# Optimization experiments

Measured on AMD Instinct MI355X. Metric: run time of the kernel, lower is better.

The kernel has to match this reference:

```python
import jax, jax.numpy as jnp
import numpy as np

HEAD_SIZE = 64


def setup_inputs() -> dict:
    key = jax.random.key(0)
    k1, k2, k3, k4 = jax.random.split(key, 4)
    B, T, E = 8, 2048, 1024
    x = jax.random.normal(k1, (B, T, E), dtype=jnp.float32)
    # nn.Linear(n_embd, head_size, bias=False) weights: [head_size, n_embd]
    s = 1.0 / np.sqrt(E)
    Wk = jax.random.uniform(k2, (HEAD_SIZE, E), jnp.float32, -s, s)
    Wq = jax.random.uniform(k3, (HEAD_SIZE, E), jnp.float32, -s, s)
    Wv = jax.random.uniform(k4, (HEAD_SIZE, E), jnp.float32, -s, s)
    return {"x": x, "Wk": Wk, "Wq": Wq, "Wv": Wv}


def reference(x, Wk, Wq, Wv):
    # x: [B, T, E]; W*: [D, E] with D = head_size
    B, T, E = x.shape
    k = jnp.einsum("bte,de->btd", x, Wk)  # [B,T,D]
    q = jnp.einsum("bte,de->btd", x, Wq)
    v = jnp.einsum("bte,de->btd", x, Wv)
    scale = k.shape[-1] ** -0.5
    wei = jnp.einsum("btd,bsd->bts", q, k) * scale  # [B,T,T]
    causal = jnp.tril(jnp.ones((T, T), dtype=bool))
    wei = jnp.where(causal, wei, -jnp.inf)
    wei = jax.nn.softmax(wei, axis=-1)
    # dropout p=0.0 (eval): identity
    return jnp.einsum("bts,bsd->btd", wei, v)
```

## Files before the change

### kernel.cpp

```cpp
#include <hip/hip_runtime.h>
#include <hip/hip_bf16.h>


typedef __bf16 bf16x8 __attribute__((ext_vector_type(8)));
typedef float  f32x4  __attribute__((ext_vector_type(4)));

#define T_SEQ 2048
#define E_DIM 1024
#define D_HEAD 64
#define M_TOT 16384
#define NSPLIT 4
#define SC_LOG2E 0.18033688011112042f

#define BAR() asm volatile("s_barrier" ::: "memory")
#define WAITVM(N) do { asm volatile("s_waitcnt vmcnt(" #N ")" ::: "memory"); \
                       __builtin_amdgcn_sched_barrier(0); } while (0)

__device__ __forceinline__ unsigned short f2b(float f) {
  union { float f; unsigned int u; } cv; cv.f = f;
  unsigned int u = cv.u;
  u += 0x7FFFu + ((u >> 16) & 1u);
  return (unsigned short)(u >> 16);
}

__device__ __forceinline__ unsigned int f2b2(float a, float b) {
#if __has_builtin(__builtin_amdgcn_cvt_pk_bf16_f32)
  typedef __bf16 bf16x2_t __attribute__((ext_vector_type(2)));
  union { bf16x2_t v; unsigned int u; } cv;
  cv.v = __builtin_amdgcn_cvt_pk_bf16_f32(a, b);
  return cv.u;
#else
  return (unsigned int)f2b(a) | ((unsigned int)f2b(b) << 16);
#endif
}

__device__ __forceinline__ void dma16(const void* g, void* l) {
  __builtin_amdgcn_global_load_lds(
      (const __attribute__((address_space(1))) void*)g,
      (__attribute__((address_space(3))) void*)l, 16, 0, 0);
}

__global__ __launch_bounds__(256) void wcvt_kernel(
    const float* __restrict__ Wk, const float* __restrict__ Wq,
    const float* __restrict__ Wv, unsigned short* __restrict__ Wb)
{
  int i = blockIdx.x * 256 + threadIdx.x;
  int n = i >> 8, c4 = i & 255;
  const float* src = (n < 64) ? Wq + n * E_DIM
                   : (n < 128) ? Wk + (n - 64) * E_DIM
                               : Wv + (n - 128) * E_DIM;
  float4 v = *(const float4*)(src + c4 * 4);
  *(uint2*)(Wb + (size_t)n * E_DIM + c4 * 4) = make_uint2(f2b2(v.x, v.y), f2b2(v.z, v.w));
}

__global__ __launch_bounds__(256, 2) void proj_kernel(
    const float* __restrict__ x, const unsigned short* __restrict__ Wb,
    unsigned short* __restrict__ qws, unsigned short* __restrict__ kws,
    unsigned short* __restrict__ vtws)
{
  __shared__ __align__(16) float x_lds[2][32 * 64];
  __shared__ __align__(16) unsigned short w_lds[2][192 * 64];

  const int tid = threadIdx.x, wv = tid >> 6, lane = tid & 63;
  const int c = lane & 15, quad = lane >> 4;
  const int row0 = blockIdx.x * 32;

  auto stage = [&](int k0, int buf) {
    for (int j = 0; j < 2; ++j) {
      int base = (wv * 2 + j) * 64;
      int ci = base + lane;
      int r = ci >> 4, p = ci & 15, g = p ^ (r & 15);
      dma16(x + (size_t)(row0 + r) * E_DIM + k0 + g * 4, &x_lds[buf][base * 4]);
    }
    for (int j = 0; j < 6; ++j) {
      int base_r = (wv * 6 + j) * 8;
      int r = base_r + (lane >> 3);
      int g = (lane & 7) ^ (r & 7);
      dma16(Wb + (size_t)r * E_DIM + k0 + g * 8, &w_lds[buf][base_r * 64]);
    }
  };

  f32x4 acc[6];
  for (int j = 0; j < 6; ++j)
    for (int r = 0; r < 4; ++r) acc[j][r] = 0.0f;

  stage(0, 0);

  for (int s = 0; s < 16; ++s) {
    const int cur = s & 1;
    BAR();
    if (s < 15) { stage((s + 1) * 64, cur ^ 1); WAITVM(8); }
    else        { WAITVM(0); }
    BAR();

    for (int ks = 0; ks < 2; ++ks) {
      const int g0 = ks * 8 + quad * 2;
      union { unsigned int u[4]; bf16x8 v; } A0, A1;
      {
        const int m = c;
        f32x4 v1 = *(const f32x4*)&x_lds[cur][m * 64 + ((g0 ^ (m & 15)) << 2)];
        f32x4 v2 = *(const f32x4*)&x_lds[cur][m * 64 + (((g0 + 1) ^ (m & 15)) << 2)];
        A0.u[0] = f2b2(v1[0], v1[1]); A0.u[1] = f2b2(v1[2], v1[3]);
        A0.u[2] = f2b2(v2[0], v2[1]); A0.u[3] = f2b2(v2[2], v2[3]);
      }
      {
        const int m = 16 + c;
        f32x4 v1 = *(const f32x4*)&x_lds[cur][m * 64 + ((g0 ^ (m & 15)) << 2)];
        f32x4 v2 = *(const f32x4*)&x_lds[cur][m * 64 + (((g0 + 1) ^ (m & 15)) << 2)];
        A1.u[0] = f2b2(v1[0], v1[1]); A1.u[1] = f2b2(v1[2], v1[3]);
        A1.u[2] = f2b2(v2[0], v2[1]); A1.u[3] = f2b2(v2[2], v2[3]);
      }
      for (int j = 0; j < 3; ++j) {
        const int n = (wv * 3 + j) * 16 + c;
        bf16x8 bb = *(const bf16x8*)&w_lds[cur][n * 64 + (((ks * 4 + quad) ^ (n & 7)) << 3)];
        acc[j * 2]     = __builtin_amdgcn_mfma_f32_16x16x32_bf16(A0.v, bb, acc[j * 2], 0, 0, 0);
        acc[j * 2 + 1] = __builtin_amdgcn_mfma_f32_16x16x32_bf16(A1.v, bb, acc[j * 2 + 1], 0, 0, 0);
      }
    }
  }

  for (int mt = 0; mt < 2; ++mt) {
    const int rbase = row0 + mt * 16 + quad * 4;
    for (int j = 0; j < 3; ++j) {
      const int nt = wv * 3 + j;
      const f32x4 a = acc[j * 2 + mt];
      if (nt < 4) {
        int d = nt * 16 + c;
        for (int r = 0; r < 4; ++r)
          qws[(size_t)(rbase + r) * D_HEAD + d] = f2b(a[r] * SC_LOG2E);
      } else if (nt < 8) {
        int d = (nt - 4) * 16 + c;
        for (int r = 0; r < 4; ++r)
          kws[(size_t)(rbase + r) * D_HEAD + d] = f2b(a[r]);
      } else {
        int d = (nt - 8) * 16 + c;
        int bb = rbase >> 11, tt = rbase & 2047;
        *(ushort4*)&vtws[(size_t)bb * D_HEAD * T_SEQ + (size_t)d * T_SEQ + tt] =
            make_ushort4(f2b(a[0]), f2b(a[1]), f2b(a[2]), f2b(a[3]));
      }
    }
  }
}

__global__ __launch_bounds__(256, 4) void attn_kernel(
    const unsigned short* __restrict__ qws, const unsigned short* __restrict__ kws,
    const unsigned short* __restrict__ vtws,
    unsigned short* __restrict__ opart, float* __restrict__ lpart)
{
  __shared__ __align__(16) unsigned short k_lds[2 * 64 * 64];
  __shared__ __align__(16) unsigned short v_lds[2 * 64 * 64];
  __shared__ __align__(16) unsigned short p_lds[64 * 64];

  const int tid = threadIdx.x, wv = tid >> 6, lane = tid & 63;
  const int c = lane & 15, quad = lane >> 4;
  const int qi = blockIdx.x, b = blockIdx.y, sg = blockIdx.z;
  const int qt = ((sg ^ b) & 1) ? qi : 31 - qi;
  const int t0 = qt * 64;
  const size_t qkb = (size_t)b * T_SEQ * D_HEAD;
  const size_t vtb = (size_t)b * D_HEAD * T_SEQ;
  const int niter = (qt >= sg) ? ((qt - sg) >> 2) + 1 : 0;
  if (niter == 0) return;

  const int rloc = wv * 16 + quad * 4;
  const size_t prow = ((size_t)sg * 8 + b) * T_SEQ;

  const int mrow = wv * 16 + c;
  const bf16x8 qf0 = *(const bf16x8*)(qws + qkb + (size_t)(t0 + mrow) * D_HEAD + quad * 8);
  const bf16x8 qf1 = *(const bf16x8*)(qws + qkb + (size_t)(t0 + mrow) * D_HEAD + 32 + quad * 8);

  bf16x8 ones;
  { union { unsigned short s[8]; bf16x8 v; } o;
    for (int i = 0; i < 8; ++i) o.s[i] = 0x3F80;
    ones = o.v; }

  f32x4 acc_o[4], acc_l;
  for (int r = 0; r < 4; ++r) acc_l[r] = 0.0f;
  for (int nt = 0; nt < 4; ++nt)
    for (int r = 0; r < 4; ++r) acc_o[nt][r] = 0.0f;

  auto stageKV = [&](int s0, int buf) {
    unsigned short* kb = k_lds + buf * 4096;
    unsigned short* vb = v_lds + buf * 4096;
    for (int j = 0; j < 2; ++j) {
      int base = (wv * 2 + j) * 64;
      int p = base + lane;
      int r = p >> 3, g = (p & 7) ^ (r & 7);
      dma16(kws + qkb + (size_t)(s0 + r) * D_HEAD + g * 8, kb + base * 8);
    }
    for (int j = 0; j < 2; ++j) {
      int base = (wv * 2 + j) * 64;
      int p = base + lane;
      int r = p >> 3, g = (p & 7) ^ (r & 7);
      dma16(vtws + vtb + (size_t)r * T_SEQ + s0 + g * 8, vb + base * 8);
    }
  };

  const bool mydiag = (sg == (qt & 3));
  stageKV(sg * 64, 0);

  for (int it = 0; it < niter; ++it) {
    const int s0 = (sg + 4 * it) * 64;
    const int cur = it & 1;
    BAR();
    if (it + 1 < niter) { stageKV((sg + 4 * (it + 1)) * 64, cur ^ 1); WAITVM(4); }
    else                { WAITVM(0); }
    BAR();

    const unsigned short* kb = k_lds + cur * 4096;
    const unsigned short* vb = v_lds + cur * 4096;

    f32x4 accs[4];
    for (int nt = 0; nt < 4; ++nt)
      for (int r = 0; r < 4; ++r) accs[nt][r] = 0.0f;
    for (int nt = 0; nt < 4; ++nt) {
      int n = nt * 16 + c;
      bf16x8 kf0 = *(const bf16x8*)&kb[n * 64 + ((quad ^ (n & 7)) << 3)];
      bf16x8 kf1 = *(const bf16x8*)&kb[n * 64 + (((4 + quad) ^ (n & 7)) << 3)];
      accs[nt] = __builtin_amdgcn_mfma_f32_16x16x32_bf16(qf0, kf0, accs[nt], 0, 0, 0);
      accs[nt] = __builtin_amdgcn_mfma_f32_16x16x32_bf16(qf1, kf1, accs[nt], 0, 0, 0);
    }
    if (mydiag && it == niter - 1) {
      for (int nt = 0; nt < 4; ++nt) {
        int scol = s0 + nt * 16 + c;
        for (int r = 0; r < 4; ++r)
          if (scol > t0 + rloc + r) accs[nt][r] = -__builtin_inff();
      }
    }

    for (int nt = 0; nt < 4; ++nt)
      for (int r = 0; r < 4; ++r)
        accs[nt][r] = __builtin_exp2f(accs[nt][r]);

    for (int nt = 0; nt < 4; ++nt) {
      unsigned int u01 = f2b2(accs[nt][0], accs[nt][1]);
      unsigned int u23 = f2b2(accs[nt][2], accs[nt][3]);
      const int X = nt * 2 + (c >> 3), cl = c & 7;
      const int r0 = rloc, r1 = rloc + 1, r2 = rloc + 2, r3 = rloc + 3;
      p_lds[r0 * 64 + ((X ^ (r0 & 7)) << 3) + cl] = (unsigned short)u01;
      p_lds[r1 * 64 + ((X ^ (r1 & 7)) << 3) + cl] = (unsigned short)(u01 >> 16);
      p_lds[r2 * 64 + ((X ^ (r2 & 7)) << 3) + cl] = (unsigned short)u23;
      p_lds[r3 * 64 + ((X ^ (r3 & 7)) << 3) + cl] = (unsigned short)(u23 >> 16);
    }

    for (int ks = 0; ks < 2; ++ks) {
      int kg = ks * 4 + quad;
      bf16x8 pf = *(const bf16x8*)&p_lds[mrow * 64 + ((kg ^ (mrow & 7)) << 3)];
      acc_l = __builtin_amdgcn_mfma_f32_16x16x32_bf16(pf, ones, acc_l, 0, 0, 0);
      for (int nt = 0; nt < 4; ++nt) {
        int n = nt * 16 + c;
        bf16x8 vv = *(const bf16x8*)&vb[n * 64 + ((kg ^ (n & 7)) << 3)];
        acc_o[nt] = __builtin_amdgcn_mfma_f32_16x16x32_bf16(pf, vv, acc_o[nt], 0, 0, 0);
      }
    }
  }

  for (int nt = 0; nt < 4; ++nt)
    for (int r = 0; r < 4; ++r)
      opart[(prow + t0 + rloc + r) * D_HEAD + nt * 16 + c] = f2b(acc_o[nt][r]);
  if (c == 0)
    for (int r = 0; r < 4; ++r) lpart[prow + t0 + rloc + r] = acc_l[r];
}

__global__ __launch_bounds__(256) void merge_kernel(
    const unsigned short* __restrict__ opart, const float* __restrict__ lpart,
    float* __restrict__ out)
{
  int gid = blockIdx.x * 256 + threadIdx.x;
  int gr = gid >> 4, d4 = (gid & 15) * 4;
  const int jmax = (gr & 2047) >> 6;
  float L = 0.0f;
  float4 o = make_float4(0.f, 0.f, 0.f, 0.f);
  for (int i = 0; i < NSPLIT; ++i) {
    if (i > jmax) break;
    L += lpart[(size_t)i * M_TOT + gr];
    ushort4 u = *(const ushort4*)(opart + (size_t)i * M_TOT * D_HEAD + (size_t)gr * D_HEAD + d4);
    union { unsigned int u; float f; } cx, cy, cz, cw;
    cx.u = (unsigned int)u.x << 16; cy.u = (unsigned int)u.y << 16;
    cz.u = (unsigned int)u.z << 16; cw.u = (unsigned int)u.w << 16;
    o.x += cx.f; o.y += cy.f; o.z += cz.f; o.w += cw.f;
  }
  float inv = 1.0f / L;
  o.x *= inv; o.y *= inv; o.z *= inv; o.w *= inv;
  *(float4*)(out + (size_t)gr * D_HEAD + d4) = o;
}

extern "C" void kernel_launch(void* const* d_in, const int* in_sizes, int n_in,
                              void* d_out, int out_size, void* d_ws, size_t ws_size,
                              hipStream_t stream) {
  const float* x  = (const float*)d_in[0];
  const float* Wk = (const float*)d_in[1];
  const float* Wq = (const float*)d_in[2];
  const float* Wv = (const float*)d_in[3];
  float* out = (float*)d_out;

  unsigned short* qws   = (unsigned short*)d_ws;
  unsigned short* kws   = qws + (size_t)M_TOT * D_HEAD;
  unsigned short* vtws  = kws + (size_t)M_TOT * D_HEAD;
  unsigned short* Wb    = vtws + (size_t)M_TOT * D_HEAD;
  unsigned short* opart = Wb + 192 * E_DIM;
  float* lpart = (float*)(opart + (size_t)NSPLIT * M_TOT * D_HEAD);

  wcvt_kernel<<<192, 256, 0, stream>>>(Wk, Wq, Wv, Wb);
  proj_kernel<<<M_TOT / 32, 256, 0, stream>>>(x, Wb, qws, kws, vtws);
  attn_kernel<<<dim3(32, 8, NSPLIT), 256, 0, stream>>>(qws, kws, vtws, opart, lpart);
  merge_kernel<<<M_TOT * 16 / 256, 256, 0, stream>>>(opart, lpart, out);
}
```

Measured before the change: 134.7 us.

## Fuse all four kernels into one cooperative persistent kernel with grid syncs

Replaces the four separate launches (weight convert, projection, split attention, merge) with one cooperative kernel of 512 blocks that runs each phase in turn, separated by grid.sync(). The attention phase loops over two work units per block to cover the 1024 tiles. The intent is to remove per-launch overhead and the gaps between kernels. In exchange it adds grid-wide barrier costs, fixes the grid at 512 blocks, which limits load balancing in the attention phase, and keeps the old four-launch path as a fallback if the cooperative launch fails.

```diff
diff --git a/kernel.cpp b/kernel.cpp
--- a/kernel.cpp
+++ b/kernel.cpp
@@ -1,5 +1,8 @@
 #include <hip/hip_runtime.h>
 #include <hip/hip_bf16.h>
+#include <hip/hip_cooperative_groups.h>
+
+namespace cg = cooperative_groups;
 
 
 typedef __bf16 bf16x8 __attribute__((ext_vector_type(8)));
@@ -38,6 +41,258 @@
   __builtin_amdgcn_global_load_lds(
       (const __attribute__((address_space(1))) void*)g,
       (__attribute__((address_space(3))) void*)l, 16, 0, 0);
+}
+
+__global__ __launch_bounds__(256, 2) void fused_kernel(
+    const float* __restrict__ x, const float* __restrict__ Wk,
+    const float* __restrict__ Wq, const float* __restrict__ Wv,
+    unsigned short* __restrict__ qws, unsigned short* __restrict__ kws,
+    unsigned short* __restrict__ vtws, unsigned short* __restrict__ Wb,
+    unsigned short* __restrict__ opart, float* __restrict__ lpart,
+    float* __restrict__ out)
+{
+  __shared__ __align__(16) unsigned char lds_raw[40960];
+  cg::grid_group grid = cg::this_grid();
+
+  const int tid = threadIdx.x, bid = blockIdx.x;
+  const int wv = tid >> 6, lane = tid & 63;
+  const int c = lane & 15, quad = lane >> 4;
+
+  {
+    int i = bid * 256 + tid;
+    if (i < 49152) {
+      int n = i >> 8, c4 = i & 255;
+      const float* src = (n < 64) ? Wq + n * E_DIM
+                       : (n < 128) ? Wk + (n - 64) * E_DIM
+                                   : Wv + (n - 128) * E_DIM;
+      float4 v = *(const float4*)(src + c4 * 4);
+      *(uint2*)(Wb + (size_t)n * E_DIM + c4 * 4) =
+          make_uint2(f2b2(v.x, v.y), f2b2(v.z, v.w));
+    }
+  }
+  grid.sync();
+
+  {
+    float*          x_lds = (float*)lds_raw;
+    unsigned short* w_lds = (unsigned short*)(lds_raw + 8192);
+    const int row0 = bid * 32;
+
+    auto stage = [&](int k0, int buf) {
+      {
+        int base = wv * 64;
+        int ci = base + lane;
+        int r = ci >> 3, p = ci & 7, g = p ^ (r & 7);
+        dma16(x + (size_t)(row0 + r) * E_DIM + k0 + g * 4,
+              x_lds + buf * 1024 + base * 4);
+      }
+      for (int j = 0; j < 3; ++j) {
+        int base = (wv * 3 + j) * 64;
+        int ci = base + lane;
+        int r = ci >> 2, p = ci & 3, g = p ^ ((r ^ (r >> 2)) & 3);
+        dma16(Wb + (size_t)r * E_DIM + k0 + g * 8,
+              w_lds + buf * 6144 + base * 8);
+      }
+    };
+
+    f32x4 acc[6];
+    for (int j = 0; j < 6; ++j)
+      for (int r = 0; r < 4; ++r) acc[j][r] = 0.0f;
+
+    stage(0, 0);
+
+    for (int s = 0; s < 32; ++s) {
+      const int cur = s & 1;
+      BAR();
+      if (s < 31) { stage((s + 1) * 32, cur ^ 1); WAITVM(4); }
+      else        { WAITVM(0); }
+      BAR();
+
+      const int g0 = quad * 2;
+      union { unsigned int u[4]; bf16x8 v; } A0, A1;
+      {
+        const int m = c;
+        f32x4 v1 = *(const f32x4*)&x_lds[cur * 1024 + m * 32 + ((g0 ^ (m & 7)) << 2)];
+        f32x4 v2 = *(const f32x4*)&x_lds[cur * 1024 + m * 32 + (((g0 + 1) ^ (m & 7)) << 2)];
+        A0.u[0] = f2b2(v1[0], v1[1]); A0.u[1] = f2b2(v1[2], v1[3]);
+        A0.u[2] = f2b2(v2[0], v2[1]); A0.u[3] = f2b2(v2[2], v2[3]);
+      }
+      {
+        const int m = 16 + c;
+        f32x4 v1 = *(const f32x4*)&x_lds[cur * 1024 + m * 32 + ((g0 ^ (m & 7)) << 2)];
+        f32x4 v2 = *(const f32x4*)&x_lds[cur * 1024 + m * 32 + (((g0 + 1) ^ (m & 7)) << 2)];
+        A1.u[0] = f2b2(v1[0], v1[1]); A1.u[1] = f2b2(v1[2], v1[3]);
+        A1.u[2] = f2b2(v2[0], v2[1]); A1.u[3] = f2b2(v2[2], v2[3]);
+      }
+      for (int j = 0; j < 3; ++j) {
+        const int n = (wv * 3 + j) * 16 + c;
+        bf16x8 bb = *(const bf16x8*)&w_lds[cur * 6144 + n * 32 +
+                        ((quad ^ ((n ^ (n >> 2)) & 3)) << 3)];
+        acc[j * 2]     = __builtin_amdgcn_mfma_f32_16x16x32_bf16(A0.v, bb, acc[j * 2], 0, 0, 0);
+        acc[j * 2 + 1] = __builtin_amdgcn_mfma_f32_16x16x32_bf16(A1.v, bb, acc[j * 2 + 1], 0, 0, 0);
+      }
+    }
+
+    for (int mt = 0; mt < 2; ++mt) {
+      const int rbase = row0 + mt * 16 + quad * 4;
+      for (int j = 0; j < 3; ++j) {
+        const int nt = wv * 3 + j;
+        const f32x4 a = acc[j * 2 + mt];
+        if (nt < 4) {
+          int d = nt * 16 + c;
+          for (int r = 0; r < 4; ++r)
+            qws[(size_t)(rbase + r) * D_HEAD + d] = f2b(a[r] * SC_LOG2E);
+        } else if (nt < 8) {
+          int d = (nt - 4) * 16 + c;
+          for (int r = 0; r < 4; ++r)
+            kws[(size_t)(rbase + r) * D_HEAD + d] = f2b(a[r]);
+        } else {
+          int d = (nt - 8) * 16 + c;
+          int bb = rbase >> 11, tt = rbase & 2047;
+          *(ushort4*)&vtws[(size_t)bb * D_HEAD * T_SEQ + (size_t)d * T_SEQ + tt] =
+              make_ushort4(f2b(a[0]), f2b(a[1]), f2b(a[2]), f2b(a[3]));
+        }
+      }
+    }
+  }
+  grid.sync();
+
+  {
+    unsigned short* k_lds = (unsigned short*)lds_raw;
+    unsigned short* v_lds = (unsigned short*)(lds_raw + 16384);
+    unsigned short* p_lds = (unsigned short*)(lds_raw + 32768);
+
+    for (int u = 0; u < 2; ++u) {
+      const int uid = bid + u * 512;
+      const int qi = uid & 31, b = (uid >> 5) & 7, sg = uid >> 8;
+      const int qt = ((sg ^ b) & 1) ? qi : 31 - qi;
+      const int t0 = qt * 64;
+      const size_t qkb = (size_t)b * T_SEQ * D_HEAD;
+      const size_t vtb = (size_t)b * D_HEAD * T_SEQ;
+      const int niter = (qt >= sg) ? ((qt - sg) >> 2) + 1 : 0;
+      if (niter == 0) continue;
+
+      const int rloc = wv * 16 + quad * 4;
+      const size_t prow = ((size_t)sg * 8 + b) * T_SEQ;
+
+      const int mrow = wv * 16 + c;
+      const bf16x8 qf0 = *(const bf16x8*)(qws + qkb + (size_t)(t0 + mrow) * D_HEAD + quad * 8);
+      const bf16x8 qf1 = *(const bf16x8*)(qws + qkb + (size_t)(t0 + mrow) * D_HEAD + 32 + quad * 8);
+
+      bf16x8 ones;
+      { union { unsigned short s[8]; bf16x8 v; } o;
+        for (int i = 0; i < 8; ++i) o.s[i] = 0x3F80;
+        ones = o.v; }
+
+      f32x4 acc_o[4], acc_l;
+      for (int r = 0; r < 4; ++r) acc_l[r] = 0.0f;
+      for (int nt = 0; nt < 4; ++nt)
+        for (int r = 0; r < 4; ++r) acc_o[nt][r] = 0.0f;
+
+      auto stageKV = [&](int s0, int buf) {
+        unsigned short* kb = k_lds + buf * 4096;
+        unsigned short* vb = v_lds + buf * 4096;
+        for (int j = 0; j < 2; ++j) {
+          int base = (wv * 2 + j) * 64;
+          int p = base + lane;
+          int r = p >> 3, g = (p & 7) ^ (r & 7);
+          dma16(kws + qkb + (size_t)(s0 + r) * D_HEAD + g * 8, kb + base * 8);
+        }
+        for (int j = 0; j < 2; ++j) {
+          int base = (wv * 2 + j) * 64;
+          int p = base + lane;
+          int r = p >> 3, g = (p & 7) ^ (r & 7);
+          dma16(vtws + vtb + (size_t)r * T_SEQ + s0 + g * 8, vb + base * 8);
+        }
+      };
+
+      const bool mydiag = (sg == (qt & 3));
+      BAR();
+      stageKV(sg * 64, 0);
+
+      for (int it = 0; it < niter; ++it) {
+        const int s0 = (sg + 4 * it) * 64;
+        const int cur = it & 1;
+        BAR();
+        if (it + 1 < niter) { stageKV((sg + 4 * (it + 1)) * 64, cur ^ 1); WAITVM(4); }
+        else                { WAITVM(0); }
+        BAR();
+
+        const unsigned short* kb = k_lds + cur * 4096;
+        const unsigned short* vb = v_lds + cur * 4096;
+
+        f32x4 accs[4];
+        for (int nt = 0; nt < 4; ++nt)
+          for (int r = 0; r < 4; ++r) accs[nt][r] = 0.0f;
+        for (int nt = 0; nt < 4; ++nt) {
+          int n = nt * 16 + c;
+          bf16x8 kf0 = *(const bf16x8*)&kb[n * 64 + ((quad ^ (n & 7)) << 3)];
+          bf16x8 kf1 = *(const bf16x8*)&kb[n * 64 + (((4 + quad) ^ (n & 7)) << 3)];
+          accs[nt] = __builtin_amdgcn_mfma_f32_16x16x32_bf16(qf0, kf0, accs[nt], 0, 0, 0);
+          accs[nt] = __builtin_amdgcn_mfma_f32_16x16x32_bf16(qf1, kf1, accs[nt], 0, 0, 0);
+        }
+        if (mydiag && it == niter - 1) {
+          for (int nt = 0; nt < 4; ++nt) {
+            int scol = s0 + nt * 16 + c;
+            for (int r = 0; r < 4; ++r)
+              if (scol > t0 + rloc + r) accs[nt][r] = -__builtin_inff();
+          }
+        }
+
+        for (int nt = 0; nt < 4; ++nt)
+          for (int r = 0; r < 4; ++r)
+            accs[nt][r] = __builtin_exp2f(accs[nt][r]);
+
+        for (int nt = 0; nt < 4; ++nt) {
+          unsigned int u01 = f2b2(accs[nt][0], accs[nt][1]);
+          unsigned int u23 = f2b2(accs[nt][2], accs[nt][3]);
+          const int X = nt * 2 + (c >> 3), cl = c & 7;
+          const int r0 = rloc, r1 = rloc + 1, r2 = rloc + 2, r3 = rloc + 3;
+          p_lds[r0 * 64 + ((X ^ (r0 & 7)) << 3) + cl] = (unsigned short)u01;
+          p_lds[r1 * 64 + ((X ^ (r1 & 7)) << 3) + cl] = (unsigned short)(u01 >> 16);
+          p_lds[r2 * 64 + ((X ^ (r2 & 7)) << 3) + cl] = (unsigned short)u23;
+          p_lds[r3 * 64 + ((X ^ (r3 & 7)) << 3) + cl] = (unsigned short)(u23 >> 16);
+        }
+
+        for (int ks = 0; ks < 2; ++ks) {
+          int kg = ks * 4 + quad;
+          bf16x8 pf = *(const bf16x8*)&p_lds[mrow * 64 + ((kg ^ (mrow & 7)) << 3)];
+          acc_l = __builtin_amdgcn_mfma_f32_16x16x32_bf16(pf, ones, acc_l, 0, 0, 0);
+          for (int nt = 0; nt < 4; ++nt) {
+            int n = nt * 16 + c;
+            bf16x8 vv = *(const bf16x8*)&vb[n * 64 + ((kg ^ (n & 7)) << 3)];
+            acc_o[nt] = __builtin_amdgcn_mfma_f32_16x16x32_bf16(pf, vv, acc_o[nt], 0, 0, 0);
+          }
+        }
+      }
+
+      for (int nt = 0; nt < 4; ++nt)
+        for (int r = 0; r < 4; ++r)
+          opart[(prow + t0 + rloc + r) * D_HEAD + nt * 16 + c] = f2b(acc_o[nt][r]);
+      if (c == 0)
+        for (int r = 0; r < 4; ++r) lpart[prow + t0 + rloc + r] = acc_l[r];
+    }
+  }
+  grid.sync();
+
+  for (int ch = 0; ch < 2; ++ch) {
+    int gid = bid * 256 + tid + ch * 131072;
+    int gr = gid >> 4, d4 = (gid & 15) * 4;
+    const int jmax = (gr & 2047) >> 6;
+    float L = 0.0f;
+    float4 o = make_float4(0.f, 0.f, 0.f, 0.f);
+    for (int i = 0; i < NSPLIT; ++i) {
+      if (i > jmax) break;
+      L += lpart[(size_t)i * M_TOT + gr];
+      ushort4 u = *(const ushort4*)(opart + (size_t)i * M_TOT * D_HEAD + (size_t)gr * D_HEAD + d4);
+      union { unsigned int u; float f; } cx, cy, cz, cw;
+      cx.u = (unsigned int)u.x << 16; cy.u = (unsigned int)u.y << 16;
+      cz.u = (unsigned int)u.z << 16; cw.u = (unsigned int)u.w << 16;
+      o.x += cx.f; o.y += cy.f; o.z += cz.f; o.w += cw.f;
+    }
+    float inv = 1.0f / L;
+    o.x *= inv; o.y *= inv; o.z *= inv; o.w *= inv;
+    *(float4*)(out + (size_t)gr * D_HEAD + d4) = o;
+  }
 }
 
 __global__ __launch_bounds__(256) void wcvt_kernel(
@@ -300,8 +555,14 @@
   unsigned short* opart = Wb + 192 * E_DIM;
   float* lpart = (float*)(opart + (size_t)NSPLIT * M_TOT * D_HEAD);
 
-  wcvt_kernel<<<192, 256, 0, stream>>>(Wk, Wq, Wv, Wb);
-  proj_kernel<<<M_TOT / 32, 256, 0, stream>>>(x, Wb, qws, kws, vtws);
-  attn_kernel<<<dim3(32, 8, NSPLIT), 256, 0, stream>>>(qws, kws, vtws, opart, lpart);
-  merge_kernel<<<M_TOT * 16 / 256, 256, 0, stream>>>(opart, lpart, out);
-}
+  void* args[] = { &x, &Wk, &Wq, &Wv, &qws, &kws, &vtws, &Wb, &opart, &lpart, &out };
+  hipError_t err = hipLaunchCooperativeKernel((const void*)fused_kernel,
+                                              dim3(512), dim3(256), args, 0, stream);
+  if (err != hipSuccess) {
+    (void)hipGetLastError();
+    wcvt_kernel<<<192, 256, 0, stream>>>(Wk, Wq, Wv, Wb);
+    proj_kernel<<<M_TOT / 32, 256, 0, stream>>>(x, Wb, qws, kws, vtws);
+    attn_kernel<<<dim3(32, 8, NSPLIT), 256, 0, stream>>>(qws, kws, vtws, opart, lpart);
+    merge_kernel<<<M_TOT * 16 / 256, 256, 0, stream>>>(opart, lpart, out);
+  }
+}
```

After: 323.6 us. 140% more time.
